# Kernel tuning notes

Hardware: AMD Instinct MI355X
Metric: run time of the kernel (lower is better)

The kernel has to match this reference:

```python
import jax, jax.numpy as jnp
import numpy as np

GRID_SIZE = 5
SPLINE_ORDER = 3
GRID_RANGE = (-1.0, 1.0)
BATCH, IN_FEATURES, OUT_FEATURES = 8192, 512, 512


def make_grid():
    h = (GRID_RANGE[1] - GRID_RANGE[0]) / GRID_SIZE
    n = GRID_SIZE + 2 * SPLINE_ORDER + 1  # 12 knots
    return jnp.linspace(GRID_RANGE[0] - SPLINE_ORDER * h,
                        GRID_RANGE[1] + SPLINE_ORDER * h,
                        n, dtype=jnp.float32)


def b_spline(x, grid, k=SPLINE_ORDER):
    # Cox-de Boor recursion. x: (B, in) -> basis: (B, in, grid_size + k)
    x = x[..., None]                     # (B, in, 1)
    g = grid[None, None, :]              # (1, 1, n_knots)
    basis = ((x >= g[..., :-1]) & (x < g[..., 1:])).astype(x.dtype)
    for p in range(1, k + 1):
        left_denom = g[..., p:-1] - g[..., :-(p + 1)]
        right_denom = g[..., p + 1:] - g[..., 1:-p]
        left_denom = jnp.where(left_denom > 0, left_denom, jnp.ones_like(left_denom))
        right_denom = jnp.where(right_denom > 0, right_denom, jnp.ones_like(right_denom))
        left = (x - g[..., :-(p + 1)]) / left_denom * basis[..., :-1]
        right = (g[..., p + 1:] - x) / right_denom * basis[..., 1:]
        basis = left + right
    return basis


def setup_inputs() -> dict:
    key = jax.random.key(0)
    k1, k2, k3 = jax.random.split(key, 3)
    # x uniform in grid_range so spline basis is active
    x = jax.random.uniform(k1, (BATCH, IN_FEATURES), jnp.float32, minval=-1.0, maxval=1.0)
    # kaiming_uniform-like init for base weight
    bound = 1.0 / np.sqrt(IN_FEATURES)
    base_weight = jax.random.uniform(k2, (OUT_FEATURES, IN_FEATURES), jnp.float32,
                                     minval=-bound, maxval=bound)
    spline_weight = jax.random.normal(k3, (OUT_FEATURES, IN_FEATURES,
                                           GRID_SIZE + SPLINE_ORDER), jnp.float32) * 0.1
    return {"x": x, "base_weight": base_weight, "spline_weight": spline_weight}


def reference(x, base_weight, spline_weight):
    grid = make_grid()
    scale_base, scale_spline = 1.0, 1.0
    base_out = x @ base_weight.T                         # (B, out)
    basis = b_spline(x, grid, SPLINE_ORDER)              # (B, in, G+k)
    spline_out = jnp.einsum('bil,oil->bo', basis, spline_weight)
    return scale_base * base_out + scale_spline * spline_out
```

## Files before the change

### kernel.cpp

```cpp
#include <hip/hip_runtime.h>
#include <stdint.h>

typedef _Float16 half8 __attribute__((ext_vector_type(8)));
typedef float floatx4 __attribute__((ext_vector_type(4)));
typedef uint32_t u32x4 __attribute__((ext_vector_type(4)));

#define BM 128
#define BN 128
#define BK 64
#define NT 512
#define KT_BASE 8
#define KT_TOTAL 72
#define IF 512
#define NF 512

__device__ __forceinline__ uint32_t swz(uint32_t b) {
  return b ^ (((b >> 7) & 7u) << 4);
}

__device__ __forceinline__ uint32_t pk(float a, float b) {
  return __builtin_bit_cast(uint32_t, __builtin_amdgcn_cvt_pkrtz(a, b));
}

__global__ __launch_bounds__(NT, 2)
void kan_fused(const float* __restrict__ xg, const float* __restrict__ bwg,
               const float* __restrict__ swg, float* __restrict__ outg)
{
  __shared__ _Float16 As[BM * BK];
  __shared__ _Float16 Bs[BN * BK];

  const int tid = threadIdx.x;
  const int lane = tid & 63;
  const int wv = tid >> 6;
  const int wm = wv >> 2;
  const int wn = wv & 3;

  const int bid = blockIdx.x;
  const int lb = (bid & 7) * 32 + (bid >> 3);
  const int bm0 = (lb & 63) * BM;
  const int bn0 = (lb >> 6) * BN;

  const int rT = tid >> 3;
  const int c8 = (tid & 7) * 8;
  const int ii = tid & 7;
  const uint32_t wA0 = swz((uint32_t)rT * 128u + (uint32_t)c8 * 2u);
  const uint32_t wA1 = swz((uint32_t)(rT + 64) * 128u + (uint32_t)c8 * 2u);

  char* AsB = (char*)As;
  char* BsB = (char*)Bs;

  uint32_t rdA[4], rdB[2];
  {
    const int rr = lane & 15;
    const uint32_t cc = (uint32_t)(lane >> 4) * 16u;
#pragma unroll
    for (int mi = 0; mi < 4; ++mi)
      rdA[mi] = swz((uint32_t)(wm * 64 + mi * 16 + rr) * 128u + cc);
#pragma unroll
    for (int ni = 0; ni < 2; ++ni)
      rdB[ni] = swz((uint32_t)(wn * 32 + ni * 16 + rr) * 128u + cc);
  }

  floatx4 acc[4][2];
#pragma unroll
  for (int mi = 0; mi < 4; ++mi)
#pragma unroll
    for (int ni = 0; ni < 2; ++ni)
      acc[mi][ni] = (floatx4){0.f, 0.f, 0.f, 0.f};

  float4 aL[4];
  float4 bL[4];
  float xv0, xv1;

  auto LOAD = [&](int kt) {
    if (kt < KT_BASE) {
      const int kb = kt * 64;
      const float* a0 = xg + (size_t)(bm0 + rT) * IF + kb + c8;
      const float* a1 = a0 + (size_t)64 * IF;
      aL[0] = ((const float4*)a0)[0]; aL[1] = ((const float4*)a0)[1];
      aL[2] = ((const float4*)a1)[0]; aL[3] = ((const float4*)a1)[1];
      const float* b0 = bwg + (size_t)(bn0 + rT) * IF + kb + c8;
      const float* b1 = b0 + (size_t)64 * IF;
      bL[0] = ((const float4*)b0)[0]; bL[1] = ((const float4*)b0)[1];
      bL[2] = ((const float4*)b1)[0]; bL[3] = ((const float4*)b1)[1];
    } else {
      const int ks = (kt - KT_BASE) * 64;
      const int i0 = ks >> 3;
      xv0 = xg[(size_t)(bm0 + rT) * IF + i0 + ii];
      xv1 = xg[(size_t)(bm0 + rT + 64) * IF + i0 + ii];
      const float* b0 = swg + (size_t)(bn0 + rT) * 4096 + ks + c8;
      const float* b1 = b0 + (size_t)64 * 4096;
      bL[0] = ((const float4*)b0)[0]; bL[1] = ((const float4*)b0)[1];
      bL[2] = ((const float4*)b1)[0]; bL[3] = ((const float4*)b1)[1];
    }
  };

  auto BASIS = [&](float xv) -> u32x4 {
    float u = (xv + 2.2f) * 2.5f;
    int j = (int)u;
    j = j < 3 ? 3 : (j > 7 ? 7 : j);
    float t = u - (float)j;
    float omt = 1.0f - t;
    float t2 = t * t, t3 = t2 * t;
    const float s6 = 0.16666666666666666f;
    float w0 = omt * omt * omt * s6;
    float w1 = (3.0f * t3 - 6.0f * t2 + 4.0f) * s6;
    float w2 = (-3.0f * t3 + 3.0f * t2 + 3.0f * t + 1.0f) * s6;
    float w3 = t3 * s6;
    uint32_t c0 = pk(w0, w1);
    uint32_t c1 = pk(w2, w3);
    const int j3 = j - 3;
    const bool odd = (j3 & 1) != 0;
    uint32_t lo  = odd ? (c0 << 16) : c0;
    uint32_t mid = odd ? ((c0 >> 16) | (c1 << 16)) : c1;
    uint32_t hi  = odd ? (c1 >> 16) : 0u;
    const int wofs = j3 >> 1;
    u32x4 r;
    r.x = (wofs == 0) ? lo : 0u;
    r.y = (wofs == 0) ? mid : ((wofs == 1) ? lo : 0u);
    r.z = (wofs == 0) ? hi : ((wofs == 1) ? mid : lo);
    r.w = (wofs == 1) ? hi : ((wofs == 2) ? mid : 0u);
    return r;
  };

  auto WRITE = [&](int kt) {
    if (kt < KT_BASE) {
      u32x4 v0; v0.x = pk(aL[0].x, aL[0].y); v0.y = pk(aL[0].z, aL[0].w);
                v0.z = pk(aL[1].x, aL[1].y); v0.w = pk(aL[1].z, aL[1].w);
      u32x4 v1; v1.x = pk(aL[2].x, aL[2].y); v1.y = pk(aL[2].z, aL[2].w);
                v1.z = pk(aL[3].x, aL[3].y); v1.w = pk(aL[3].z, aL[3].w);
      *(u32x4*)(AsB + wA0) = v0;
      *(u32x4*)(AsB + wA1) = v1;
    } else {
      *(u32x4*)(AsB + wA0) = BASIS(xv0);
      *(u32x4*)(AsB + wA1) = BASIS(xv1);
    }
    u32x4 u0; u0.x = pk(bL[0].x, bL[0].y); u0.y = pk(bL[0].z, bL[0].w);
              u0.z = pk(bL[1].x, bL[1].y); u0.w = pk(bL[1].z, bL[1].w);
    u32x4 u1; u1.x = pk(bL[2].x, bL[2].y); u1.y = pk(bL[2].z, bL[2].w);
              u1.z = pk(bL[3].x, bL[3].y); u1.w = pk(bL[3].z, bL[3].w);
    *(u32x4*)(BsB + wA0) = u0;
    *(u32x4*)(BsB + wA1) = u1;
  };

  auto COMPUTE = [&]() {
#pragma unroll
    for (int kk = 0; kk < 2; ++kk) {
      const uint32_t ko = (uint32_t)(kk * 64);
      half8 a[4], b[2];
#pragma unroll
      for (int mi = 0; mi < 4; ++mi) {
        const uint32_t off = rdA[mi] ^ ko;
        a[mi] = *(const half8*)(AsB + off);
      }
#pragma unroll
      for (int ni = 0; ni < 2; ++ni) {
        const uint32_t off = rdB[ni] ^ ko;
        b[ni] = *(const half8*)(BsB + off);
      }
#pragma unroll
      for (int mi = 0; mi < 4; ++mi)
#pragma unroll
        for (int ni = 0; ni < 2; ++ni)
          acc[mi][ni] = __builtin_amdgcn_mfma_f32_16x16x32_f16(a[mi], b[ni], acc[mi][ni], 0, 0, 0);
    }
  };

  LOAD(0);
  WRITE(0);
  __syncthreads();
#pragma unroll 1
  for (int kt = 0; kt < KT_TOTAL; ++kt) {
    const bool more = (kt + 1) < KT_TOTAL;
    if (more) LOAD(kt + 1);
    COMPUTE();
    __syncthreads();
    if (more) WRITE(kt + 1);
    __syncthreads();
  }

  const int er = (lane >> 4) * 4;
  const int ec = lane & 15;
#pragma unroll
  for (int mi = 0; mi < 4; ++mi) {
#pragma unroll
    for (int ni = 0; ni < 2; ++ni) {
      const size_t base = (size_t)(bm0 + wm * 64 + mi * 16 + er) * NF
                        + (size_t)(bn0 + wn * 32 + ni * 16 + ec);
#pragma unroll
      for (int e = 0; e < 4; ++e)
        outg[base + (size_t)e * NF] = acc[mi][ni][e];
    }
  }
}

extern "C" void kernel_launch(void* const* d_in, const int* in_sizes, int n_in,
                              void* d_out, int out_size, void* d_ws, size_t ws_size,
                              hipStream_t stream) {
  const float* x  = (const float*)d_in[0];
  const float* bw = (const float*)d_in[1];
  const float* sw = (const float*)d_in[2];
  float* out = (float*)d_out;
  hipLaunchKernelGGL(kan_fused, dim3(256), dim3(NT), 0, stream, x, bw, sw, out);
}
```

Baseline: 87.44 us.

## Prepack weights to fp16 swizzled tiles and double-buffer LDS with direct global-to-LDS loads

```diff
diff --git a/kernel.cpp b/kernel.cpp
--- a/kernel.cpp
+++ b/kernel.cpp
@@ -13,6 +13,9 @@
 #define KT_TOTAL 72
 #define IF 512
 #define NF 512
+#define SW_K 4096
+#define TILE_B 16384
+#define WS_TILES (KT_TOTAL * 4)
 
 __device__ __forceinline__ uint32_t swz(uint32_t b) {
   return b ^ (((b >> 7) & 7u) << 4);
@@ -22,12 +25,35 @@
   return __builtin_bit_cast(uint32_t, __builtin_amdgcn_cvt_pkrtz(a, b));
 }
 
+__global__ __launch_bounds__(256)
+void kan_prep(const float* __restrict__ bwg, const float* __restrict__ swg,
+              uint32_t* __restrict__ wsB)
+{
+  const int gid = blockIdx.x * 256 + threadIdx.x;
+  const int T = gid >> 10;
+  const int q = gid & 1023;
+  const int kt = T >> 2;
+  const int nt = T & 3;
+  const uint32_t p = swz((uint32_t)q * 16u);
+  const int row = p >> 7;
+  const int c   = (p & 127) >> 1;
+  const int n = nt * 128 + row;
+  const float* src;
+  if (kt < KT_BASE) src = bwg + (size_t)n * IF   + kt * 64 + c;
+  else              src = swg + (size_t)n * SW_K + (kt - KT_BASE) * 64 + c;
+  float4 f0 = ((const float4*)src)[0];
+  float4 f1 = ((const float4*)src)[1];
+  u32x4 v; v.x = pk(f0.x, f0.y); v.y = pk(f0.z, f0.w);
+           v.z = pk(f1.x, f1.y); v.w = pk(f1.z, f1.w);
+  *(u32x4*)((char*)wsB + (size_t)T * TILE_B + (size_t)q * 16) = v;
+}
+
 __global__ __launch_bounds__(NT, 2)
-void kan_fused(const float* __restrict__ xg, const float* __restrict__ bwg,
-               const float* __restrict__ swg, float* __restrict__ outg)
+void kan_fused(const float* __restrict__ xg, const uint32_t* __restrict__ wsB,
+               float* __restrict__ outg)
 {
-  __shared__ _Float16 As[BM * BK];
-  __shared__ _Float16 Bs[BN * BK];
+  __shared__ _Float16 As[2][BM * BK];
+  __shared__ _Float16 Bs[2][BN * BK];
 
   const int tid = threadIdx.x;
   const int lane = tid & 63;
@@ -38,7 +64,8 @@
   const int bid = blockIdx.x;
   const int lb = (bid & 7) * 32 + (bid >> 3);
   const int bm0 = (lb & 63) * BM;
-  const int bn0 = (lb >> 6) * BN;
+  const int ntI = lb >> 6;
+  const int bn0 = ntI * BN;
 
   const int rT = tid >> 3;
   const int c8 = (tid & 7) * 8;
@@ -69,29 +96,30 @@
       acc[mi][ni] = (floatx4){0.f, 0.f, 0.f, 0.f};
 
   float4 aL[4];
-  float4 bL[4];
   float xv0, xv1;
 
-  auto LOAD = [&](int kt) {
+  auto GLOADB = [&](int kt, int nb) {
+    const char* src = (const char*)wsB + (size_t)(kt * 4 + ntI) * TILE_B + (size_t)tid * 16;
+    char* dst = BsB + nb * TILE_B + tid * 16;
+    __builtin_amdgcn_global_load_lds(
+        (const __attribute__((address_space(1))) uint32_t*)src,
+        (__attribute__((address_space(3))) uint32_t*)dst, 16, 0, 0);
+    __builtin_amdgcn_global_load_lds(
+        (const __attribute__((address_space(1))) uint32_t*)(src + 8192),
+        (__attribute__((address_space(3))) uint32_t*)(dst + 8192), 16, 0, 0);
+  };
+
+  auto LOADX = [&](int kt) {
     if (kt < KT_BASE) {
       const int kb = kt * 64;
       const float* a0 = xg + (size_t)(bm0 + rT) * IF + kb + c8;
       const float* a1 = a0 + (size_t)64 * IF;
       aL[0] = ((const float4*)a0)[0]; aL[1] = ((const float4*)a0)[1];
       aL[2] = ((const float4*)a1)[0]; aL[3] = ((const float4*)a1)[1];
-      const float* b0 = bwg + (size_t)(bn0 + rT) * IF + kb + c8;
-      const float* b1 = b0 + (size_t)64 * IF;
-      bL[0] = ((const float4*)b0)[0]; bL[1] = ((const float4*)b0)[1];
-      bL[2] = ((const float4*)b1)[0]; bL[3] = ((const float4*)b1)[1];
     } else {
-      const int ks = (kt - KT_BASE) * 64;
-      const int i0 = ks >> 3;
+      const int i0 = (kt - KT_BASE) * 8;
       xv0 = xg[(size_t)(bm0 + rT) * IF + i0 + ii];
       xv1 = xg[(size_t)(bm0 + rT + 64) * IF + i0 + ii];
-      const float* b0 = swg + (size_t)(bn0 + rT) * 4096 + ks + c8;
-      const float* b1 = b0 + (size_t)64 * 4096;
-      bL[0] = ((const float4*)b0)[0]; bL[1] = ((const float4*)b0)[1];
-      bL[2] = ((const float4*)b1)[0]; bL[3] = ((const float4*)b1)[1];
     }
   };
 
@@ -123,41 +151,34 @@
     return r;
   };
 
-  auto WRITE = [&](int kt) {
+  auto WRITEA = [&](int kt, int nb) {
+    char* base = AsB + nb * TILE_B;
     if (kt < KT_BASE) {
       u32x4 v0; v0.x = pk(aL[0].x, aL[0].y); v0.y = pk(aL[0].z, aL[0].w);
                 v0.z = pk(aL[1].x, aL[1].y); v0.w = pk(aL[1].z, aL[1].w);
       u32x4 v1; v1.x = pk(aL[2].x, aL[2].y); v1.y = pk(aL[2].z, aL[2].w);
                 v1.z = pk(aL[3].x, aL[3].y); v1.w = pk(aL[3].z, aL[3].w);
-      *(u32x4*)(AsB + wA0) = v0;
-      *(u32x4*)(AsB + wA1) = v1;
+      *(u32x4*)(base + wA0) = v0;
+      *(u32x4*)(base + wA1) = v1;
     } else {
-      *(u32x4*)(AsB + wA0) = BASIS(xv0);
-      *(u32x4*)(AsB + wA1) = BASIS(xv1);
-    }
-    u32x4 u0; u0.x = pk(bL[0].x, bL[0].y); u0.y = pk(bL[0].z, bL[0].w);
-              u0.z = pk(bL[1].x, bL[1].y); u0.w = pk(bL[1].z, bL[1].w);
-    u32x4 u1; u1.x = pk(bL[2].x, bL[2].y); u1.y = pk(bL[2].z, bL[2].w);
-              u1.z = pk(bL[3].x, bL[3].y); u1.w = pk(bL[3].z, bL[3].w);
-    *(u32x4*)(BsB + wA0) = u0;
-    *(u32x4*)(BsB + wA1) = u1;
-  };
-
-  auto COMPUTE = [&]() {
+      *(u32x4*)(base + wA0) = BASIS(xv0);
+      *(u32x4*)(base + wA1) = BASIS(xv1);
+    }
+  };
+
+  auto COMPUTE = [&](int cb) {
+    const char* ab = AsB + cb * TILE_B;
+    const char* bb = BsB + cb * TILE_B;
 #pragma unroll
     for (int kk = 0; kk < 2; ++kk) {
       const uint32_t ko = (uint32_t)(kk * 64);
       half8 a[4], b[2];
 #pragma unroll
-      for (int mi = 0; mi < 4; ++mi) {
-        const uint32_t off = rdA[mi] ^ ko;
-        a[mi] = *(const half8*)(AsB + off);
-      }
-#pragma unroll
-      for (int ni = 0; ni < 2; ++ni) {
-        const uint32_t off = rdB[ni] ^ ko;
-        b[ni] = *(const half8*)(BsB + off);
-      }
+      for (int mi = 0; mi < 4; ++mi)
+        a[mi] = *(const half8*)(ab + (rdA[mi] ^ ko));
+#pragma unroll
+      for (int ni = 0; ni < 2; ++ni)
+        b[ni] = *(const half8*)(bb + (rdB[ni] ^ ko));
 #pragma unroll
       for (int mi = 0; mi < 4; ++mi)
 #pragma unroll
@@ -166,16 +187,19 @@
     }
   };
 
-  LOAD(0);
-  WRITE(0);
+  LOADX(0);
+  GLOADB(0, 0);
+  WRITEA(0, 0);
   __syncthreads();
+
 #pragma unroll 1
   for (int kt = 0; kt < KT_TOTAL; ++kt) {
+    const int cur = kt & 1;
+    const int nxt = cur ^ 1;
     const bool more = (kt + 1) < KT_TOTAL;
-    if (more) LOAD(kt + 1);
-    COMPUTE();
-    __syncthreads();
-    if (more) WRITE(kt + 1);
+    if (more) { GLOADB(kt + 1, nxt); LOADX(kt + 1); }
+    COMPUTE(cur);
+    if (more) WRITEA(kt + 1, nxt);
     __syncthreads();
   }
 
@@ -201,5 +225,7 @@
   const float* bw = (const float*)d_in[1];
   const float* sw = (const float*)d_in[2];
   float* out = (float*)d_out;
-  hipLaunchKernelGGL(kan_fused, dim3(256), dim3(NT), 0, stream, x, bw, sw, out);
-}
+  uint32_t* wsB = (uint32_t*)d_ws;
+  hipLaunchKernelGGL(kan_prep, dim3(WS_TILES * 1024 / 256), dim3(256), 0, stream, bw, sw, wsB);
+  hipLaunchKernelGGL(kan_fused, dim3(256), dim3(NT), 0, stream, x, wsB, out);
+}
```

Measured after the change: 97.09 us. 11.0% more time.
